# Kernel optimization log

Hardware: AMD Instinct MI355X
Metric: run time of the kernel (lower is better)

Reference implementation:

```python
import jax, jax.numpy as jnp
import numpy as np

B, S, E, H, HD, M = 2, 2048, 1024, 16, 64, 2048  # batch, seq, embed, heads, head_dim, mem_width


def setup_inputs() -> dict:
    key = jax.random.key(0)
    k1, k2, k3, k4, k5 = jax.random.split(key, 5)
    tensor = jax.random.normal(k1, (B, S, E), dtype=jnp.float32)
    # QueryProj: Linear(E -> [H, HD]) with weight + bias (kaiming-style scale)
    Wq = jax.random.normal(k2, (E, H, HD), dtype=jnp.float32) / np.sqrt(E)
    bq = jnp.zeros((H, HD), dtype=jnp.float32)
    # Learnable key/value memory banks [H, M, HD]
    K = jax.random.normal(k3, (H, M, HD), dtype=jnp.float32) / np.sqrt(HD)
    V = jax.random.normal(k4, (H, M, HD), dtype=jnp.float32) / np.sqrt(HD)
    # DeheadProj: Linear([H, HD] -> E)
    Wd = jax.random.normal(k5, (H, HD, E), dtype=jnp.float32) / np.sqrt(H * HD)
    bd = jnp.zeros((E,), dtype=jnp.float32)
    return {"tensor": tensor, "Wq": Wq, "bq": bq, "K": K, "V": V, "Wd": Wd, "bd": bd}


def reference(tensor, Wq, bq, K, V, Wd, bd):
    # Head-splitting query projection: [B,S,E] -> [B,S,H,HD]
    q = jnp.einsum('bse,ehd->bshd', tensor, Wq) + bq
    # Attention logits against fixed parameter memory: [B,S,H,M]
    logits = jnp.einsum('bshd,hmd->bshm', q, K)
    score = jax.nn.softmax(logits, axis=-1)  # mode == 'softmax'
    # Value readout, scaled AFTER the matmul by sqrt(head_dim) (as in source)
    attn = jnp.einsum('bshm,hmd->bshd', score, V) / jnp.sqrt(jnp.asarray(HD, dtype=q.dtype))
    # Dehead projection back to embedding width: [B,S,E]
    out = jnp.einsum('bshd,hde->bse', attn, Wd) + bd
    return out
```

## Files before the change

### kernel.cpp

```cpp
#include <hip/hip_runtime.h>

typedef _Float16 half8 __attribute__((ext_vector_type(8)));
typedef _Float16 half4v __attribute__((ext_vector_type(4)));
typedef __fp16 fp16x2 __attribute__((ext_vector_type(2)));
typedef float f32x4 __attribute__((ext_vector_type(4)));
typedef float float4v __attribute__((ext_vector_type(4)));

constexpr int NS = 4096;
constexpr int E  = 1024;
constexpr int H  = 16;
constexpr int HD = 64;
constexpr int M  = 2048;
constexpr int HE = 1024;

__device__ __forceinline__ void gload16(const _Float16* g, _Float16* l) {
  __builtin_amdgcn_global_load_lds((__attribute__((address_space(1))) void*)g,
                                   (__attribute__((address_space(3))) void*)l, 16, 0, 0);
}

__device__ __forceinline__ float fexp2(float x) {
#if __has_builtin(__builtin_amdgcn_exp2f)
  return __builtin_amdgcn_exp2f(x);
#else
  return __expf(x * 0.6931471805599453f);
#endif
}


__global__ void cvt_f32_to_f16(const float* __restrict__ in, _Float16* __restrict__ out,
                               float scale) {
  int i = (blockIdx.x * 256 + threadIdx.x) * 4;
  float4v v = *(const float4v*)(in + i);
  half4v o = { (_Float16)(v[0] * scale), (_Float16)(v[1] * scale),
               (_Float16)(v[2] * scale), (_Float16)(v[3] * scale) };
  *(half4v*)(out + i) = o;
}

__global__ void transpose_cvt(const float* __restrict__ in, _Float16* __restrict__ out,
                              int R, int C) {
  __shared__ float tile[32][33];
  int b = blockIdx.z;
  in  += (size_t)b * R * C;
  out += (size_t)b * R * C;
  int c0 = blockIdx.x * 32, r0 = blockIdx.y * 32;
  int tx = threadIdx.x, ty = threadIdx.y;
#pragma unroll
  for (int i = 0; i < 4; ++i)
    tile[ty + 8 * i][tx] = in[(size_t)(r0 + ty + 8 * i) * C + c0 + tx];
  __syncthreads();
#pragma unroll
  for (int i = 0; i < 4; ++i)
    out[(size_t)(c0 + ty + 8 * i) * R + r0 + tx] = (_Float16)tile[tx][ty + 8 * i];
}


template <typename OUT_T>
__global__ __launch_bounds__(512, 2) void gemm_f16(
    const _Float16* __restrict__ A,
    const _Float16* __restrict__ Bt,
    const float* __restrict__ bias,
    OUT_T* __restrict__ C,
    int Ncols, int K, float scale)
{
  __shared__ alignas(16) _Float16 Ab[2][8 * 512];
  __shared__ alignas(16) _Float16 Bb[2][8 * 512];
  const int tid = threadIdx.x;
  const int wave = tid >> 6, lane = tid & 63;
  const int l15 = lane & 15, l4 = lane >> 4;

  const int nwg = gridDim.x;
  int wg = (blockIdx.x & 7) * (nwg >> 3) + (blockIdx.x >> 3);
  const int nbn = Ncols >> 7;
  const int mblk = wg / nbn, nblk = wg % nbn;

  const _Float16* aS = A  + (size_t)(mblk * 128 + wave * 16 + l15) * K + l4 * 8;
  const _Float16* bS = Bt + (size_t)(nblk * 128 + wave * 16 + l15) * K + l4 * 8;
  _Float16* aD0 = &Ab[0][wave * 512];
  _Float16* aD1 = &Ab[1][wave * 512];
  _Float16* bD0 = &Bb[0][wave * 512];
  _Float16* bD1 = &Bb[1][wave * 512];

  const int wr = wave >> 2, wc = wave & 3;
  f32x4 acc[4][2];
#pragma unroll
  for (int i = 0; i < 4; ++i)
#pragma unroll
    for (int n = 0; n < 2; ++n) acc[i][n] = (f32x4){0.f, 0.f, 0.f, 0.f};

  gload16(aS, aD0);
  gload16(bS, bD0);
  aS += 32; bS += 32;

  const int nk = K >> 5;
  for (int kt = 0; kt < nk; ++kt) {
    if (kt + 1 < nk) {
      gload16(aS, (kt & 1) ? aD0 : aD1);
      gload16(bS, (kt & 1) ? bD0 : bD1);
      aS += 32; bS += 32;
      asm volatile("s_waitcnt vmcnt(2)" ::: "memory");
    } else {
      asm volatile("s_waitcnt vmcnt(0)" ::: "memory");
    }
    __builtin_amdgcn_s_barrier();
    const _Float16* Ac = (kt & 1) ? &Ab[1][0] : &Ab[0][0];
    const _Float16* Bc = (kt & 1) ? &Bb[1][0] : &Bb[0][0];
    half8 af[4], bf[2];
#pragma unroll
    for (int i = 0; i < 4; ++i) af[i] = *(const half8*)(Ac + (wr * 4 + i) * 512 + lane * 8);
#pragma unroll
    for (int n = 0; n < 2; ++n) bf[n] = *(const half8*)(Bc + (wc * 2 + n) * 512 + lane * 8);
    __builtin_amdgcn_s_setprio(1);
#pragma unroll
    for (int i = 0; i < 4; ++i)
#pragma unroll
      for (int n = 0; n < 2; ++n)
        acc[i][n] = __builtin_amdgcn_mfma_f32_16x16x32_f16(af[i], bf[n], acc[i][n], 0, 0, 0);
    __builtin_amdgcn_s_setprio(0);
    asm volatile("s_waitcnt lgkmcnt(0)" ::: "memory");
    __builtin_amdgcn_sched_barrier(0);
    __builtin_amdgcn_s_barrier();
  }

  const int row0 = mblk * 128 + wr * 64;
  const int col0 = nblk * 128 + wc * 32;
#pragma unroll
  for (int n = 0; n < 2; ++n) {
    int col = col0 + n * 16 + l15;
    float bv = bias[col];
#pragma unroll
    for (int i = 0; i < 4; ++i)
#pragma unroll
      for (int r = 0; r < 4; ++r) {
        int row = row0 + i * 16 + l4 * 4 + r;
        C[(size_t)row * Ncols + col] = (OUT_T)(acc[i][n][r] * scale + bv);
      }
  }
}


__global__ __launch_bounds__(256, 2) void attn_fused(
    const _Float16* __restrict__ qh,
    const _Float16* __restrict__ Kh,
    const _Float16* __restrict__ Vth,
    _Float16* __restrict__ attnh)
{
  __shared__ alignas(16) _Float16 Kb[2][4096];
  __shared__ alignas(16) _Float16 Vb[2][4096];
  __shared__ alignas(16) _Float16 Pl[4096];

  int wg = (blockIdx.x & 7) * 64 + (blockIdx.x >> 3);
  const int h = wg >> 5, sblk = wg & 31;
  const int tid = threadIdx.x;
  const int wave = tid >> 6, lane = tid & 63, l15 = lane & 15, l4 = lane >> 4;
  const int s0 = sblk * 128 + wave * 32;

  half8 qf[2][2];
#pragma unroll
  for (int f = 0; f < 2; ++f) {
    const _Float16* qp = qh + (size_t)(s0 + f * 16 + l15) * HE + h * HD + l4 * 8;
    qf[f][0] = *(const half8*)qp;
    qf[f][1] = *(const half8*)(qp + 32);
  }

  const _Float16* kSrc = Kh + (size_t)h * M * HD
                         + (size_t)((wave >> 1) * 16 + l15) * HD + (wave & 1) * 32 + l4 * 8;
  const _Float16* vSrc = Vth + (size_t)h * HD * M + (size_t)(wave * 16 + l15) * M + l4 * 8;
  const int dOff = wave * 512 + lane * 8;

  _Float16* Pw = &Pl[wave * 1024];
  const int pAddr = (l4 >> 1) * 128 + l15 * 8 + (l4 & 1) * 4;

  half8 vones;
#pragma unroll
  for (int j = 0; j < 8; ++j) vones[j] = (_Float16)1.0f;

  f32x4 acc[2][4];
  f32x4 accs[2];
#pragma unroll
  for (int f = 0; f < 2; ++f) {
    accs[f] = (f32x4){0.f, 0.f, 0.f, 0.f};
#pragma unroll
    for (int n = 0; n < 4; ++n) acc[f][n] = (f32x4){0.f, 0.f, 0.f, 0.f};
  }

#define STAGE(b, m0) {                                          \
    gload16(kSrc + (size_t)(m0) * HD,        &Kb[b][dOff]);     \
    gload16(kSrc + (size_t)((m0) + 32) * HD, &Kb[b][dOff + 2048]); \
    gload16(vSrc + (m0),                     &Vb[b][dOff]);     \
    gload16(vSrc + (m0) + 32,                &Vb[b][dOff + 2048]); }

#define CHALF(b, hh) {                                                                     \
    const _Float16* Kc = &Kb[b][(hh) * 2048];                                              \
    const _Float16* Vc = &Vb[b][(hh) * 2048];                                              \
    half8 kf[4], vf[4];                                                                    \
    _Pragma("unroll")                                                                      \
    for (int c = 0; c < 4; ++c) {                                                          \
      kf[c] = *(const half8*)(Kc + c * 512 + lane * 8);                                    \
      vf[c] = *(const half8*)(Vc + c * 512 + lane * 8);                                    \
    }                                                                                      \
    f32x4 z = (f32x4){0.f, 0.f, 0.f, 0.f};                                                 \
    f32x4 s[2][2];                                                                         \
    __builtin_amdgcn_s_setprio(1);                                                         \
    _Pragma("unroll")                                                                      \
    for (int f = 0; f < 2; ++f)                                                            \
      _Pragma("unroll")                                                                    \
      for (int t = 0; t < 2; ++t) {                                                        \
        s[f][t] = __builtin_amdgcn_mfma_f32_16x16x32_f16(kf[t * 2 + 0], qf[f][0], z, 0, 0, 0); \
        s[f][t] = __builtin_amdgcn_mfma_f32_16x16x32_f16(kf[t * 2 + 1], qf[f][1], s[f][t], 0, 0, 0); \
      }                                                                                    \
    __builtin_amdgcn_s_setprio(0);                                                         \
    _Pragma("unroll")                                                                      \
    for (int f = 0; f < 2; ++f)                                                            \
      _Pragma("unroll")                                                                    \
      for (int t = 0; t < 2; ++t) {                                                        \
        fp16x2 lo = __builtin_amdgcn_cvt_pkrtz(fexp2(s[f][t][0]), fexp2(s[f][t][1]));      \
        fp16x2 hi = __builtin_amdgcn_cvt_pkrtz(fexp2(s[f][t][2]), fexp2(s[f][t][3]));      \
        *(fp16x2*)(Pw + pAddr + f * 512 + t * 256)     = lo;                               \
        *(fp16x2*)(Pw + pAddr + f * 512 + t * 256 + 2) = hi;                               \
      }                                                                                    \
    asm volatile("s_waitcnt lgkmcnt(0)" ::: "memory");                                     \
    __builtin_amdgcn_sched_barrier(0);                                                     \
    half8 pf0 = *(const half8*)(Pw + lane * 8);                                            \
    half8 pf1 = *(const half8*)(Pw + 512 + lane * 8);                                      \
    __builtin_amdgcn_s_setprio(1);                                                         \
    _Pragma("unroll")                                                                      \
    for (int n = 0; n < 4; ++n) {                                                          \
      acc[0][n] = __builtin_amdgcn_mfma_f32_16x16x32_f16(pf0, vf[n], acc[0][n], 0, 0, 0);  \
      acc[1][n] = __builtin_amdgcn_mfma_f32_16x16x32_f16(pf1, vf[n], acc[1][n], 0, 0, 0);  \
    }                                                                                      \
    accs[0] = __builtin_amdgcn_mfma_f32_16x16x32_f16(pf0, vones, accs[0], 0, 0, 0);        \
    accs[1] = __builtin_amdgcn_mfma_f32_16x16x32_f16(pf1, vones, accs[1], 0, 0, 0);        \
    __builtin_amdgcn_s_setprio(0);                                                         \
  }

  STAGE(0, 0);
  for (int kt = 0; kt < 32; ++kt) {
    const int cur = kt & 1;
    if (kt < 31) {
      STAGE(cur ^ 1, (kt + 1) * 64);
      asm volatile("s_waitcnt vmcnt(4)" ::: "memory");
    } else {
      asm volatile("s_waitcnt vmcnt(0)" ::: "memory");
    }
    __builtin_amdgcn_s_barrier();
    CHALF(cur, 0);
    CHALF(cur, 1);
    __builtin_amdgcn_s_barrier();
  }

#pragma unroll
  for (int f = 0; f < 2; ++f) {
    f32x4 inv;
#pragma unroll
    for (int r = 0; r < 4; ++r) inv[r] = 1.0f / accs[f][r];
#pragma unroll
    for (int n = 0; n < 4; ++n)
#pragma unroll
      for (int r = 0; r < 4; ++r) {
        int row = s0 + f * 16 + l4 * 4 + r;
        attnh[(size_t)row * HE + h * HD + n * 16 + l15] = (_Float16)(acc[f][n][r] * inv[r]);
      }
  }
#undef STAGE
#undef CHALF
}


extern "C" void kernel_launch(void* const* d_in, const int* in_sizes, int n_in,
                              void* d_out, int out_size, void* d_ws, size_t ws_size,
                              hipStream_t stream) {
  const float* tensor = (const float*)d_in[0];
  const float* Wq     = (const float*)d_in[1];
  const float* bq     = (const float*)d_in[2];
  const float* Kp     = (const float*)d_in[3];
  const float* Vp     = (const float*)d_in[4];
  const float* Wd     = (const float*)d_in[5];
  const float* bd     = (const float*)d_in[6];
  float* out = (float*)d_out;

  char* ws = (char*)d_ws;
  _Float16* th    = (_Float16*)(ws);
  _Float16* qhb   = (_Float16*)(ws + (8  << 20));
  _Float16* attnh = (_Float16*)(ws + (16 << 20));
  _Float16* Wqt   = (_Float16*)(ws + (24 << 20));
  _Float16* Wdt   = (_Float16*)(ws + (26 << 20));
  _Float16* Khb   = (_Float16*)(ws + (28 << 20));
  _Float16* Vth   = (_Float16*)(ws + (32 << 20));

  cvt_f32_to_f16<<<(NS * E) / 1024, 256, 0, stream>>>(tensor, th, 1.0f);
  cvt_f32_to_f16<<<(H * M * HD) / 1024, 256, 0, stream>>>(Kp, Khb, 1.44269504088896f);
  transpose_cvt<<<dim3(32, 32, 1), dim3(32, 8), 0, stream>>>(Wq, Wqt, 1024, 1024);
  transpose_cvt<<<dim3(32, 32, 1), dim3(32, 8), 0, stream>>>(Wd, Wdt, 1024, 1024);
  transpose_cvt<<<dim3(2, 64, 16), dim3(32, 8), 0, stream>>>(Vp, Vth, 2048, 64);

  gemm_f16<_Float16><<<256, 512, 0, stream>>>(th, Wqt, bq, qhb, HE, E, 1.0f);
  attn_fused<<<512, 256, 0, stream>>>(qhb, Khb, Vth, attnh);
  gemm_f16<float><<<256, 512, 0, stream>>>(attnh, Wdt, bd, out, E, HE, 0.125f);
}
```

Measured before the change: 125.1 us.

## Split attention over memory halves, shrink GEMM tiles, merge weight transposes

The attention kernel now splits the memory dimension into two halves, producing 1024 workgroups that write unnormalized partial outputs and row sums. A new combine kernel adds the halves and normalizes them. The GEMMs switch to 128x64 tiles with 512 workgroups and a higher occupancy hint, and the two weight transposes run as one launch. The goal is to fill more compute units on a 256-CU part, at the cost of an extra launch and extra global traffic for the partial results.

```diff
diff --git a/kernel.cpp b/kernel.cpp
--- a/kernel.cpp
+++ b/kernel.cpp
@@ -53,9 +53,25 @@
     out[(size_t)(c0 + ty + 8 * i) * R + r0 + tx] = (_Float16)tile[tx][ty + 8 * i];
 }
 
+__global__ void transpose_cvt2(const float* __restrict__ inA, const float* __restrict__ inB,
+                               _Float16* __restrict__ outA, _Float16* __restrict__ outB) {
+  __shared__ float tile[32][33];
+  const float* in = blockIdx.z ? inB : inA;
+  _Float16* out = blockIdx.z ? outB : outA;
+  int c0 = blockIdx.x * 32, r0 = blockIdx.y * 32;
+  int tx = threadIdx.x, ty = threadIdx.y;
+#pragma unroll
+  for (int i = 0; i < 4; ++i)
+    tile[ty + 8 * i][tx] = in[(size_t)(r0 + ty + 8 * i) * 1024 + c0 + tx];
+  __syncthreads();
+#pragma unroll
+  for (int i = 0; i < 4; ++i)
+    out[(size_t)(c0 + ty + 8 * i) * 1024 + r0 + tx] = (_Float16)tile[tx][ty + 8 * i];
+}
+
 
 template <typename OUT_T>
-__global__ __launch_bounds__(512, 2) void gemm_f16(
+__global__ __launch_bounds__(512, 4) void gemm_f16(
     const _Float16* __restrict__ A,
     const _Float16* __restrict__ Bt,
     const float* __restrict__ bias,
@@ -63,55 +79,56 @@
     int Ncols, int K, float scale)
 {
   __shared__ alignas(16) _Float16 Ab[2][8 * 512];
-  __shared__ alignas(16) _Float16 Bb[2][8 * 512];
+  __shared__ alignas(16) _Float16 Bb[2][4 * 512];
   const int tid = threadIdx.x;
   const int wave = tid >> 6, lane = tid & 63;
   const int l15 = lane & 15, l4 = lane >> 4;
 
   const int nwg = gridDim.x;
   int wg = (blockIdx.x & 7) * (nwg >> 3) + (blockIdx.x >> 3);
-  const int nbn = Ncols >> 7;
+  const int nbn = Ncols >> 6;
   const int mblk = wg / nbn, nblk = wg % nbn;
 
   const _Float16* aS = A  + (size_t)(mblk * 128 + wave * 16 + l15) * K + l4 * 8;
-  const _Float16* bS = Bt + (size_t)(nblk * 128 + wave * 16 + l15) * K + l4 * 8;
+  const _Float16* bS = Bt + (size_t)(nblk * 64 + (wave & 3) * 16 + l15) * K + l4 * 8;
   _Float16* aD0 = &Ab[0][wave * 512];
   _Float16* aD1 = &Ab[1][wave * 512];
-  _Float16* bD0 = &Bb[0][wave * 512];
-  _Float16* bD1 = &Bb[1][wave * 512];
-
-  const int wr = wave >> 2, wc = wave & 3;
-  f32x4 acc[4][2];
-#pragma unroll
-  for (int i = 0; i < 4; ++i)
+  _Float16* bD0 = &Bb[0][(wave & 3) * 512];
+  _Float16* bD1 = &Bb[1][(wave & 3) * 512];
+
+  const int wr = wave >> 1, wc = wave & 1;
+  f32x4 acc[2][2];
+#pragma unroll
+  for (int i = 0; i < 2; ++i)
 #pragma unroll
     for (int n = 0; n < 2; ++n) acc[i][n] = (f32x4){0.f, 0.f, 0.f, 0.f};
 
   gload16(aS, aD0);
-  gload16(bS, bD0);
+  if (wave < 4) gload16(bS, bD0);
   aS += 32; bS += 32;
 
   const int nk = K >> 5;
   for (int kt = 0; kt < nk; ++kt) {
     if (kt + 1 < nk) {
       gload16(aS, (kt & 1) ? aD0 : aD1);
-      gload16(bS, (kt & 1) ? bD0 : bD1);
+      if (wave < 4) gload16(bS, (kt & 1) ? bD0 : bD1);
       aS += 32; bS += 32;
-      asm volatile("s_waitcnt vmcnt(2)" ::: "memory");
+      if (wave < 4) { asm volatile("s_waitcnt vmcnt(2)" ::: "memory"); }
+      else          { asm volatile("s_waitcnt vmcnt(1)" ::: "memory"); }
     } else {
       asm volatile("s_waitcnt vmcnt(0)" ::: "memory");
     }
     __builtin_amdgcn_s_barrier();
     const _Float16* Ac = (kt & 1) ? &Ab[1][0] : &Ab[0][0];
     const _Float16* Bc = (kt & 1) ? &Bb[1][0] : &Bb[0][0];
-    half8 af[4], bf[2];
-#pragma unroll
-    for (int i = 0; i < 4; ++i) af[i] = *(const half8*)(Ac + (wr * 4 + i) * 512 + lane * 8);
+    half8 af[2], bf[2];
+#pragma unroll
+    for (int i = 0; i < 2; ++i) af[i] = *(const half8*)(Ac + (wr * 2 + i) * 512 + lane * 8);
 #pragma unroll
     for (int n = 0; n < 2; ++n) bf[n] = *(const half8*)(Bc + (wc * 2 + n) * 512 + lane * 8);
     __builtin_amdgcn_s_setprio(1);
 #pragma unroll
-    for (int i = 0; i < 4; ++i)
+    for (int i = 0; i < 2; ++i)
 #pragma unroll
       for (int n = 0; n < 2; ++n)
         acc[i][n] = __builtin_amdgcn_mfma_f32_16x16x32_f16(af[i], bf[n], acc[i][n], 0, 0, 0);
@@ -121,14 +138,14 @@
     __builtin_amdgcn_s_barrier();
   }
 
-  const int row0 = mblk * 128 + wr * 64;
-  const int col0 = nblk * 128 + wc * 32;
+  const int row0 = mblk * 128 + wr * 32;
+  const int col0 = nblk * 64 + wc * 32;
 #pragma unroll
   for (int n = 0; n < 2; ++n) {
     int col = col0 + n * 16 + l15;
     float bv = bias[col];
 #pragma unroll
-    for (int i = 0; i < 4; ++i)
+    for (int i = 0; i < 2; ++i)
 #pragma unroll
       for (int r = 0; r < 4; ++r) {
         int row = row0 + i * 16 + l4 * 4 + r;
@@ -138,18 +155,21 @@
 }
 
 
-__global__ __launch_bounds__(256, 2) void attn_fused(
+__global__ __launch_bounds__(256, 4) void attn_fused(
     const _Float16* __restrict__ qh,
     const _Float16* __restrict__ Kh,
     const _Float16* __restrict__ Vth,
-    _Float16* __restrict__ attnh)
+    _Float16* __restrict__ Op0,
+    _Float16* __restrict__ Op1,
+    float* __restrict__ Spart)
 {
   __shared__ alignas(16) _Float16 Kb[2][4096];
   __shared__ alignas(16) _Float16 Vb[2][4096];
   __shared__ alignas(16) _Float16 Pl[4096];
 
-  int wg = (blockIdx.x & 7) * 64 + (blockIdx.x >> 3);
-  const int h = wg >> 5, sblk = wg & 31;
+  int wg = (blockIdx.x & 7) * 128 + (blockIdx.x >> 3);
+  const int h = wg >> 6, half = (wg >> 5) & 1, sblk = wg & 31;
+  const int m0 = half * 1024;
   const int tid = threadIdx.x;
   const int wave = tid >> 6, lane = tid & 63, l15 = lane & 15, l4 = lane >> 4;
   const int s0 = sblk * 128 + wave * 32;
@@ -183,11 +203,11 @@
     for (int n = 0; n < 4; ++n) acc[f][n] = (f32x4){0.f, 0.f, 0.f, 0.f};
   }
 
-#define STAGE(b, m0) {                                          \
-    gload16(kSrc + (size_t)(m0) * HD,        &Kb[b][dOff]);     \
-    gload16(kSrc + (size_t)((m0) + 32) * HD, &Kb[b][dOff + 2048]); \
-    gload16(vSrc + (m0),                     &Vb[b][dOff]);     \
-    gload16(vSrc + (m0) + 32,                &Vb[b][dOff + 2048]); }
+#define STAGE(b, mm) {                                          \
+    gload16(kSrc + (size_t)(mm) * HD,        &Kb[b][dOff]);     \
+    gload16(kSrc + (size_t)((mm) + 32) * HD, &Kb[b][dOff + 2048]); \
+    gload16(vSrc + (mm),                     &Vb[b][dOff]);     \
+    gload16(vSrc + (mm) + 32,                &Vb[b][dOff + 2048]); }
 
 #define CHALF(b, hh) {                                                                     \
     const _Float16* Kc = &Kb[b][(hh) * 2048];                                              \
@@ -233,11 +253,11 @@
     __builtin_amdgcn_s_setprio(0);                                                         \
   }
 
-  STAGE(0, 0);
-  for (int kt = 0; kt < 32; ++kt) {
+  STAGE(0, m0);
+  for (int kt = 0; kt < 16; ++kt) {
     const int cur = kt & 1;
-    if (kt < 31) {
-      STAGE(cur ^ 1, (kt + 1) * 64);
+    if (kt < 15) {
+      STAGE(cur ^ 1, m0 + (kt + 1) * 64);
       asm volatile("s_waitcnt vmcnt(4)" ::: "memory");
     } else {
       asm volatile("s_waitcnt vmcnt(0)" ::: "memory");
@@ -248,21 +268,41 @@
     __builtin_amdgcn_s_barrier();
   }
 
+  _Float16* Op = half ? Op1 : Op0;
+  float* Sp = Spart + (size_t)half * (NS * H);
 #pragma unroll
   for (int f = 0; f < 2; ++f) {
-    f32x4 inv;
-#pragma unroll
-    for (int r = 0; r < 4; ++r) inv[r] = 1.0f / accs[f][r];
 #pragma unroll
     for (int n = 0; n < 4; ++n)
 #pragma unroll
       for (int r = 0; r < 4; ++r) {
         int row = s0 + f * 16 + l4 * 4 + r;
-        attnh[(size_t)row * HE + h * HD + n * 16 + l15] = (_Float16)(acc[f][n][r] * inv[r]);
+        Op[(size_t)row * HE + h * HD + n * 16 + l15] = (_Float16)acc[f][n][r];
       }
+    if (l15 == 0) {
+#pragma unroll
+      for (int r = 0; r < 4; ++r) {
+        int row = s0 + f * 16 + l4 * 4 + r;
+        Sp[(size_t)row * H + h] = accs[f][r];
+      }
+    }
   }
 #undef STAGE
 #undef CHALF
+}
+
+__global__ void attn_combine(const _Float16* __restrict__ O0, const _Float16* __restrict__ O1,
+                             const float* __restrict__ Spart, _Float16* __restrict__ out) {
+  int idx = (blockIdx.x * 256 + threadIdx.x) * 8;
+  int row = idx >> 10, he = idx & 1023, h = he >> 6;
+  half8 a = *(const half8*)(O0 + idx);
+  half8 b = *(const half8*)(O1 + idx);
+  float s = Spart[(size_t)row * H + h] + Spart[(size_t)(NS + row) * H + h];
+  float inv = 1.0f / s;
+  half8 o;
+#pragma unroll
+  for (int j = 0; j < 8; ++j) o[j] = (_Float16)(((float)a[j] + (float)b[j]) * inv);
+  *(half8*)(out + idx) = o;
 }
 
 
@@ -286,14 +326,17 @@
   _Float16* Wdt   = (_Float16*)(ws + (26 << 20));
   _Float16* Khb   = (_Float16*)(ws + (28 << 20));
   _Float16* Vth   = (_Float16*)(ws + (32 << 20));
+  _Float16* Op0   = (_Float16*)(ws);
+  _Float16* Op1   = (_Float16*)(ws + (36 << 20));
+  float*    Spart = (float*)(ws + (24 << 20));
 
   cvt_f32_to_f16<<<(NS * E) / 1024, 256, 0, stream>>>(tensor, th, 1.0f);
   cvt_f32_to_f16<<<(H * M * HD) / 1024, 256, 0, stream>>>(Kp, Khb, 1.44269504088896f);
-  transpose_cvt<<<dim3(32, 32, 1), dim3(32, 8), 0, stream>>>(Wq, Wqt, 1024, 1024);
-  transpose_cvt<<<dim3(32, 32, 1), dim3(32, 8), 0, stream>>>(Wd, Wdt, 1024, 1024);
+  transpose_cvt2<<<dim3(32, 32, 2), dim3(32, 8), 0, stream>>>(Wq, Wd, Wqt, Wdt);
   transpose_cvt<<<dim3(2, 64, 16), dim3(32, 8), 0, stream>>>(Vp, Vth, 2048, 64);
 
-  gemm_f16<_Float16><<<256, 512, 0, stream>>>(th, Wqt, bq, qhb, HE, E, 1.0f);
-  attn_fused<<<512, 256, 0, stream>>>(qhb, Khb, Vth, attnh);
-  gemm_f16<float><<<256, 512, 0, stream>>>(attnh, Wdt, bd, out, E, HE, 0.125f);
-}
+  gemm_f16<_Float16><<<512, 512, 0, stream>>>(th, Wqt, bq, qhb, HE, E, 1.0f);
+  attn_fused<<<1024, 256, 0, stream>>>(qhb, Khb, Vth, Op0, Op1, Spart);
+  attn_combine<<<(NS * HE) / 2048, 256, 0, stream>>>(Op0, Op1, Spart, attnh);
+  gemm_f16<float><<<512, 512, 0, stream>>>(attnh, Wdt, bd, out, E, HE, 0.125f);
+}
```

Result: faster. 120.9 us (-3.3%).
